# Kernel tuning notes

Measured on AMD Instinct MI355X. Metric: run time of the kernel, lower is better.

## Reference

```python
import jax, jax.numpy as jnp
import numpy as np

N_NODES = 50000
N_EDGES = 500000
D_IN = 256
D_OUT = 256


def setup_inputs() -> dict:
    key = jax.random.key(0)
    ks = jax.random.split(key, 16)
    inp = {
        "features": jax.random.normal(ks[0], (N_NODES, D_IN), dtype=jnp.float32),
        "src0": jax.random.randint(ks[1], (N_EDGES,), 0, N_NODES, dtype=jnp.int64),
        "dst0": jax.random.randint(ks[2], (N_EDGES,), 0, N_NODES, dtype=jnp.int64),
        "src1": jax.random.randint(ks[3], (N_EDGES,), 0, N_NODES, dtype=jnp.int64),
        "dst1": jax.random.randint(ks[4], (N_EDGES,), 0, N_NODES, dtype=jnp.int64),
        "src2": jax.random.randint(ks[5], (N_EDGES,), 0, N_NODES, dtype=jnp.int64),
        "dst2": jax.random.randint(ks[6], (N_EDGES,), 0, N_NODES, dtype=jnp.int64),
    }
    scale = 1.0 / np.sqrt(D_IN)
    for i in range(3):
        inp[f"W{i}"] = jax.random.uniform(ks[7 + 2 * i], (D_IN, D_OUT), dtype=jnp.float32, minval=-scale, maxval=scale)
        inp[f"b{i}"] = jax.random.uniform(ks[8 + 2 * i], (D_OUT,), dtype=jnp.float32, minval=-scale, maxval=scale)
    return inp


def _relation(features, W, b, src, dst, n_nodes):
    # per-relation linear projection: [N, D_out]
    Wh = features @ W + b
    # copy_u: gather projected source features along edges -> [E, D_out]
    msg = Wh[src]
    # mean reduce onto destination nodes
    s = jax.ops.segment_sum(msg, dst, num_segments=n_nodes)
    cnt = jax.ops.segment_sum(jnp.ones((src.shape[0],), features.dtype), dst, num_segments=n_nodes)
    return s / jnp.maximum(cnt, 1.0)[:, None]


def reference(features, src0, dst0, src1, dst1, src2, dst2, W0, b0, W1, b1, W2, b2):
    n = features.shape[0]
    # multi_update_all(..., 'sum'): sum per-relation mean-aggregated messages
    h = (_relation(features, W0, b0, src0, dst0, n)
         + _relation(features, W1, b1, src1, dst1, n)
         + _relation(features, W2, b2, src2, dst2, n))
    return jax.nn.relu(h)
```

## Files before the change

kernel.cpp:

```cpp
#include <hip/hip_runtime.h>
#include <hip/hip_bf16.h>

#define N_NODES 50000
#define N_EDGES 500000
#define D 256
#define N_TOT 768
#define SCAN_N (3 * N_NODES)
#define NMB ((N_NODES + 255) / 256)
#define SLOTS 32
#define OVF_CAP 2048

typedef __attribute__((ext_vector_type(8))) __bf16 bf16x8;
typedef __attribute__((ext_vector_type(4))) float f32x4;

__device__ __forceinline__ unsigned short f2bf(float f) {
    unsigned u = __builtin_bit_cast(unsigned, f);
    u += 0x7FFFu + ((u >> 16) & 1u);
    return (unsigned short)(u >> 16);
}
__device__ __forceinline__ float bf2f(unsigned short h) {
    return __builtin_bit_cast(float, (unsigned)h << 16);
}
__device__ __forceinline__ void gload16(const unsigned short* g, __bf16* l) {
    __builtin_amdgcn_global_load_lds(
        (const __attribute__((address_space(1))) void*)g,
        (__attribute__((address_space(3))) void*)l, 16, 0, 0);
}

__global__ void prep_kernel(const float* __restrict__ feat, unsigned short* __restrict__ fb,
                            const float* __restrict__ W0, const float* __restrict__ W1,
                            const float* __restrict__ W2, unsigned short* __restrict__ WT,
                            const int* __restrict__ s0, const int* __restrict__ d0,
                            const int* __restrict__ s1, const int* __restrict__ d1,
                            const int* __restrict__ s2, const int* __restrict__ d2,
                            int* __restrict__ cur, unsigned short* __restrict__ eidx,
                            int* __restrict__ ovfc, int* __restrict__ ovf) {
    int i = blockIdx.x * blockDim.x + threadIdx.x;
    if (i < N_NODES * D / 4) {
        float4 v = ((const float4*)feat)[i];
        ushort4 pk;
        pk.x = f2bf(v.x); pk.y = f2bf(v.y); pk.z = f2bf(v.z); pk.w = f2bf(v.w);
        ((ushort4*)fb)[i] = pk;
    }
    if (i < N_TOT * D) {
        int j = i >> 8, k = i & 255;
        int r = j >> 8, c = j & 255;
        const float* W = (r == 0) ? W0 : (r == 1) ? W1 : W2;
        WT[i] = f2bf(W[k * D + c]);
    }
    if (i < 3 * N_EDGES) {
        int r = i / N_EDGES;
        int e = i - r * N_EDGES;
        const int* d = (r == 0) ? d0 : (r == 1) ? d1 : d2;
        const int* s = (r == 0) ? s0 : (r == 1) ? s1 : s2;
        int x = r * N_NODES + d[e];
        int rank = atomicAdd(&cur[x], 1);
        if (rank < SLOTS) {
            eidx[(size_t)x * SLOTS + rank] = (unsigned short)s[e];
        } else {
            int op = atomicAdd(ovfc, 1);
            if (op < OVF_CAP) { ovf[2 * op] = x; ovf[2 * op + 1] = s[e]; }
        }
    }
}

__global__ __launch_bounds__(512) void gemm_kernel(
    const unsigned short* __restrict__ A, const unsigned short* __restrict__ BT,
    const float* __restrict__ b0, const float* __restrict__ b1, const float* __restrict__ b2,
    unsigned short* __restrict__ Wh) {
    __shared__ __bf16 Asl[2][256][64];
    __shared__ __bf16 Bsl[2][256][64];
    int tid = threadIdx.x;
    int lane = tid & 63, w = tid >> 6;
    int wr = w >> 2, wc = w & 3;
    int m0 = blockIdx.x * 256;
    int p = blockIdx.y;
    const float* bp = (p == 0) ? b0 : (p == 1) ? b1 : b2;
    f32x4 acc[8][4] = {};

    auto stage = [&](int kt, int b) {
        #pragma unroll
        for (int i = 0; i < 4; ++i) {
            int slot = i * 512 + w * 64 + lane;
            int row = slot >> 3, ks = slot & 7;
            int g = ks ^ (row & 7);
            int gm = m0 + row; if (gm >= N_NODES) gm = N_NODES - 1;
            gload16(A + (size_t)gm * D + kt * 64 + g * 8,
                    &Asl[b][0][0] + (size_t)slot * 8);
            gload16(BT + (size_t)(p * 256 + row) * D + kt * 64 + g * 8,
                    &Bsl[b][0][0] + (size_t)slot * 8);
        }
    };

    stage(0, 0);
    int rr = lane & 15, q = lane >> 4;
    #pragma unroll
    for (int kt = 0; kt < 4; ++kt) {
        asm volatile("s_waitcnt vmcnt(0)" ::: "memory");
        __builtin_amdgcn_s_barrier();
        int b = kt & 1;
        if (kt + 1 < 4) stage(kt + 1, b ^ 1);
        #pragma unroll
        for (int kh = 0; kh < 2; ++kh) {
            bf16x8 af[8], bfr[4];
            #pragma unroll
            for (int mf = 0; mf < 8; ++mf) {
                int row = wr * 128 + mf * 16 + rr;
                int sl = (kh * 4 + q) ^ (row & 7);
                af[mf] = *(const bf16x8*)(&Asl[b][row][0] + sl * 8);
            }
            #pragma unroll
            for (int nf = 0; nf < 4; ++nf) {
                int row = wc * 64 + nf * 16 + rr;
                int sl = (kh * 4 + q) ^ (row & 7);
                bfr[nf] = *(const bf16x8*)(&Bsl[b][row][0] + sl * 8);
            }
            #pragma unroll
            for (int mf = 0; mf < 8; ++mf)
                #pragma unroll
                for (int nf = 0; nf < 4; ++nf)
                    acc[mf][nf] = __builtin_amdgcn_mfma_f32_16x16x32_bf16(af[mf], bfr[nf], acc[mf][nf], 0, 0, 0);
        }
        __builtin_amdgcn_s_barrier();
    }

    #pragma unroll
    for (int mf = 0; mf < 8; ++mf) {
        #pragma unroll
        for (int nf = 0; nf < 4; ++nf) {
            int col = wc * 64 + nf * 16 + rr;
            float bb = bp[col];
            #pragma unroll
            for (int reg = 0; reg < 4; ++reg) {
                int row = m0 + wr * 128 + mf * 16 + q * 4 + reg;
                if (row < N_NODES)
                    Wh[(size_t)row * N_TOT + p * 256 + col] = f2bf(acc[mf][nf][reg] + bb);
            }
        }
    }
}

__global__ void agg_kernel(const unsigned short* __restrict__ Wh, const int* __restrict__ cur,
                           const unsigned short* __restrict__ eidx, const int* __restrict__ ovfc,
                           const int* __restrict__ ovf, float* __restrict__ out) {
    int n = (blockIdx.x * blockDim.x + threadIdx.x) >> 6;
    int lane = threadIdx.x & 63;
    if (n >= N_NODES) return;

    int dg3[3], e3[3];
    #pragma unroll
    for (int r = 0; r < 3; ++r)
        dg3[r] = cur[r * N_NODES + n];
    #pragma unroll
    for (int r = 0; r < 3; ++r) {
        int x = r * N_NODES + n;
        e3[r] = (lane < min(dg3[r], SLOTS)) ? (int)eidx[(size_t)x * SLOTS + lane] : 0;
    }

    float o0 = 0.f, o1 = 0.f, o2 = 0.f, o3 = 0.f;
    #pragma unroll
    for (int r = 0; r < 3; ++r) {
        const unsigned short* whl = Wh + r * 256 + lane * 4;
        int deg = dg3[r];
        int m = min(deg, SLOTS);
        int e = e3[r];
        float4 acc = make_float4(0.f, 0.f, 0.f, 0.f);
        int j = 0;
        for (; j + 7 < m; j += 8) {
            int t0 = __shfl(e, j + 0), t1 = __shfl(e, j + 1), t2 = __shfl(e, j + 2), t3 = __shfl(e, j + 3);
            int t4 = __shfl(e, j + 4), t5 = __shfl(e, j + 5), t6 = __shfl(e, j + 6), t7 = __shfl(e, j + 7);
            ushort4 v0 = *(const ushort4*)(whl + (size_t)t0 * N_TOT);
            ushort4 v1 = *(const ushort4*)(whl + (size_t)t1 * N_TOT);
            ushort4 v2 = *(const ushort4*)(whl + (size_t)t2 * N_TOT);
            ushort4 v3 = *(const ushort4*)(whl + (size_t)t3 * N_TOT);
            ushort4 v4 = *(const ushort4*)(whl + (size_t)t4 * N_TOT);
            ushort4 v5 = *(const ushort4*)(whl + (size_t)t5 * N_TOT);
            ushort4 v6 = *(const ushort4*)(whl + (size_t)t6 * N_TOT);
            ushort4 v7 = *(const ushort4*)(whl + (size_t)t7 * N_TOT);
            acc.x += ((bf2f(v0.x) + bf2f(v1.x)) + (bf2f(v2.x) + bf2f(v3.x))) + ((bf2f(v4.x) + bf2f(v5.x)) + (bf2f(v6.x) + bf2f(v7.x)));
            acc.y += ((bf2f(v0.y) + bf2f(v1.y)) + (bf2f(v2.y) + bf2f(v3.y))) + ((bf2f(v4.y) + bf2f(v5.y)) + (bf2f(v6.y) + bf2f(v7.y)));
            acc.z += ((bf2f(v0.z) + bf2f(v1.z)) + (bf2f(v2.z) + bf2f(v3.z))) + ((bf2f(v4.z) + bf2f(v5.z)) + (bf2f(v6.z) + bf2f(v7.z)));
            acc.w += ((bf2f(v0.w) + bf2f(v1.w)) + (bf2f(v2.w) + bf2f(v3.w))) + ((bf2f(v4.w) + bf2f(v5.w)) + (bf2f(v6.w) + bf2f(v7.w)));
        }
        for (; j < m; ++j) {
            int t = __shfl(e, j);
            ushort4 v = *(const ushort4*)(whl + (size_t)t * N_TOT);
            acc.x += bf2f(v.x); acc.y += bf2f(v.y); acc.z += bf2f(v.z); acc.w += bf2f(v.w);
        }
        if (deg > SLOTS) {
            int x = r * N_NODES + n;
            int nov = min(*ovfc, OVF_CAP);
            for (int i2 = 0; i2 < nov; ++i2) {
                if (ovf[2 * i2] == x) {
                    ushort4 v = *(const ushort4*)(whl + (size_t)ovf[2 * i2 + 1] * N_TOT);
                    acc.x += bf2f(v.x); acc.y += bf2f(v.y); acc.z += bf2f(v.z); acc.w += bf2f(v.w);
                }
            }
        }
        float sc = (deg > 0) ? 1.0f / (float)deg : 0.0f;
        o0 += acc.x * sc; o1 += acc.y * sc; o2 += acc.z * sc; o3 += acc.w * sc;
    }
    f32x4 o;
    o.x = fmaxf(o0, 0.0f); o.y = fmaxf(o1, 0.0f);
    o.z = fmaxf(o2, 0.0f); o.w = fmaxf(o3, 0.0f);
    __builtin_nontemporal_store(o, (f32x4*)(out + (size_t)n * D + lane * 4));
}

extern "C" void kernel_launch(void* const* d_in, const int* in_sizes, int n_in,
                              void* d_out, int out_size, void* d_ws, size_t ws_size,
                              hipStream_t stream) {
    const float* feat = (const float*)d_in[0];
    const int* src0 = (const int*)d_in[1];
    const int* dst0 = (const int*)d_in[2];
    const int* src1 = (const int*)d_in[3];
    const int* dst1 = (const int*)d_in[4];
    const int* src2 = (const int*)d_in[5];
    const int* dst2 = (const int*)d_in[6];
    const float* W0 = (const float*)d_in[7];
    const float* b0 = (const float*)d_in[8];
    const float* W1 = (const float*)d_in[9];
    const float* b1 = (const float*)d_in[10];
    const float* W2 = (const float*)d_in[11];
    const float* b2 = (const float*)d_in[12];
    float* out = (float*)d_out;

    char* ws = (char*)d_ws;
    size_t o = 0;
    auto alloc = [&](size_t bytes) {
        size_t r = o;
        o += (bytes + 255) & ~(size_t)255;
        return r;
    };
    int* cur            = (int*)(ws + alloc((size_t)SCAN_N * 4));
    int* ovfc           = (int*)(ws + alloc(4 + (size_t)OVF_CAP * 8));
    int* ovf            = ovfc + 1;
    unsigned short* eidx = (unsigned short*)(ws + alloc((size_t)SCAN_N * SLOTS * 2));
    unsigned short* WT  = (unsigned short*)(ws + alloc((size_t)N_TOT * D * 2));
    unsigned short* fb  = (unsigned short*)(ws + alloc((size_t)N_NODES * D * 2));
    unsigned short* Wh  = (unsigned short*)(ws + alloc((size_t)N_NODES * N_TOT * 2));

    (void)hipMemsetAsync(cur, 0, (size_t)SCAN_N * 4 + 256, stream);
    prep_kernel<<<(N_NODES * D / 4 + 255) / 256, 256, 0, stream>>>(
        feat, fb, W0, W1, W2, WT,
        src0, dst0, src1, dst1, src2, dst2, cur, eidx, ovfc, ovf);
    dim3 gg(NMB, 3);
    gemm_kernel<<<gg, 512, 0, stream>>>(fb, WT, b0, b1, b2, Wh);
    agg_kernel<<<(N_NODES * 64 + 255) / 256, 256, 0, stream>>>(Wh, cur, eidx, ovfc, ovf, out);
}
```

Before: 271.2 us.

## Overlap edge bucketing with GEMM via extra specialized waves in gemm kernel

The atomic edge-bucketing work moves out of the prep kernel and into four extra wavefronts added to each GEMM workgroup, which grows from 512 to 768 threads. Those extra waves process a contiguous chunk of edge jobs in 8 sub-chunks. After each sub-chunk they issue a barrier, so their barrier count matches the 8 barriers of the MFMA waves. The goal is to hide the latency-bound scattered atomics behind the compute-bound GEMM instead of running them serially in prep. In exchange, the larger workgroup lowers the per-thread register budget for the MFMA waves, which hold large accumulators and may spill. The scheme also relies on both wave groups hitting exactly the same number of barriers.

```diff
diff --git a/kernel.cpp b/kernel.cpp
--- a/kernel.cpp
+++ b/kernel.cpp
@@ -7,6 +7,10 @@
 #define N_TOT 768
 #define SCAN_N (3 * N_NODES)
 #define NMB ((N_NODES + 255) / 256)
+#define NBLK (NMB * 3)
+#define JOBS (3 * N_EDGES)
+#define JPB ((JOBS + NBLK - 1) / NBLK)
+#define CPB ((JPB + 7) / 8)
 #define SLOTS 32
 #define OVF_CAP 2048
 
@@ -29,12 +33,7 @@
 
 __global__ void prep_kernel(const float* __restrict__ feat, unsigned short* __restrict__ fb,
                             const float* __restrict__ W0, const float* __restrict__ W1,
-                            const float* __restrict__ W2, unsigned short* __restrict__ WT,
-                            const int* __restrict__ s0, const int* __restrict__ d0,
-                            const int* __restrict__ s1, const int* __restrict__ d1,
-                            const int* __restrict__ s2, const int* __restrict__ d2,
-                            int* __restrict__ cur, unsigned short* __restrict__ eidx,
-                            int* __restrict__ ovfc, int* __restrict__ ovf) {
+                            const float* __restrict__ W2, unsigned short* __restrict__ WT) {
     int i = blockIdx.x * blockDim.x + threadIdx.x;
     if (i < N_NODES * D / 4) {
         float4 v = ((const float4*)feat)[i];
@@ -48,94 +47,113 @@
         const float* W = (r == 0) ? W0 : (r == 1) ? W1 : W2;
         WT[i] = f2bf(W[k * D + c]);
     }
-    if (i < 3 * N_EDGES) {
-        int r = i / N_EDGES;
-        int e = i - r * N_EDGES;
-        const int* d = (r == 0) ? d0 : (r == 1) ? d1 : d2;
-        const int* s = (r == 0) ? s0 : (r == 1) ? s1 : s2;
-        int x = r * N_NODES + d[e];
-        int rank = atomicAdd(&cur[x], 1);
-        if (rank < SLOTS) {
-            eidx[(size_t)x * SLOTS + rank] = (unsigned short)s[e];
-        } else {
-            int op = atomicAdd(ovfc, 1);
-            if (op < OVF_CAP) { ovf[2 * op] = x; ovf[2 * op + 1] = s[e]; }
-        }
-    }
-}
-
-__global__ __launch_bounds__(512) void gemm_kernel(
+}
+
+__global__ __launch_bounds__(768) void gemm_kernel(
     const unsigned short* __restrict__ A, const unsigned short* __restrict__ BT,
     const float* __restrict__ b0, const float* __restrict__ b1, const float* __restrict__ b2,
-    unsigned short* __restrict__ Wh) {
+    unsigned short* __restrict__ Wh,
+    const int* __restrict__ s0, const int* __restrict__ d0,
+    const int* __restrict__ s1, const int* __restrict__ d1,
+    const int* __restrict__ s2, const int* __restrict__ d2,
+    int* __restrict__ cur, unsigned short* __restrict__ eidx,
+    int* __restrict__ ovfc, int* __restrict__ ovf) {
     __shared__ __bf16 Asl[2][256][64];
     __shared__ __bf16 Bsl[2][256][64];
     int tid = threadIdx.x;
-    int lane = tid & 63, w = tid >> 6;
-    int wr = w >> 2, wc = w & 3;
-    int m0 = blockIdx.x * 256;
-    int p = blockIdx.y;
-    const float* bp = (p == 0) ? b0 : (p == 1) ? b1 : b2;
-    f32x4 acc[8][4] = {};
-
-    auto stage = [&](int kt, int b) {
+    int bid = blockIdx.y * NMB + blockIdx.x;
+
+    if (tid < 512) {
+        int lane = tid & 63, w = tid >> 6;
+        int wr = w >> 2, wc = w & 3;
+        int m0 = blockIdx.x * 256;
+        int p = blockIdx.y;
+        const float* bp = (p == 0) ? b0 : (p == 1) ? b1 : b2;
+        f32x4 acc[8][4] = {};
+
+        auto stage = [&](int kt, int b) {
+            #pragma unroll
+            for (int i = 0; i < 4; ++i) {
+                int slot = i * 512 + w * 64 + lane;
+                int row = slot >> 3, ks = slot & 7;
+                int g = ks ^ (row & 7);
+                int gm = m0 + row; if (gm >= N_NODES) gm = N_NODES - 1;
+                gload16(A + (size_t)gm * D + kt * 64 + g * 8,
+                        &Asl[b][0][0] + (size_t)slot * 8);
+                gload16(BT + (size_t)(p * 256 + row) * D + kt * 64 + g * 8,
+                        &Bsl[b][0][0] + (size_t)slot * 8);
+            }
+        };
+
+        stage(0, 0);
+        int rr = lane & 15, q = lane >> 4;
         #pragma unroll
-        for (int i = 0; i < 4; ++i) {
-            int slot = i * 512 + w * 64 + lane;
-            int row = slot >> 3, ks = slot & 7;
-            int g = ks ^ (row & 7);
-            int gm = m0 + row; if (gm >= N_NODES) gm = N_NODES - 1;
-            gload16(A + (size_t)gm * D + kt * 64 + g * 8,
-                    &Asl[b][0][0] + (size_t)slot * 8);
-            gload16(BT + (size_t)(p * 256 + row) * D + kt * 64 + g * 8,
-                    &Bsl[b][0][0] + (size_t)slot * 8);
-        }
-    };
-
-    stage(0, 0);
-    int rr = lane & 15, q = lane >> 4;
-    #pragma unroll
-    for (int kt = 0; kt < 4; ++kt) {
-        asm volatile("s_waitcnt vmcnt(0)" ::: "memory");
-        __builtin_amdgcn_s_barrier();
-        int b = kt & 1;
-        if (kt + 1 < 4) stage(kt + 1, b ^ 1);
+        for (int kt = 0; kt < 4; ++kt) {
+            asm volatile("s_waitcnt vmcnt(0)" ::: "memory");
+            __builtin_amdgcn_s_barrier();
+            int b = kt & 1;
+            if (kt + 1 < 4) stage(kt + 1, b ^ 1);
+            #pragma unroll
+            for (int kh = 0; kh < 2; ++kh) {
+                bf16x8 af[8], bfr[4];
+                #pragma unroll
+                for (int mf = 0; mf < 8; ++mf) {
+                    int row = wr * 128 + mf * 16 + rr;
+                    int sl = (kh * 4 + q) ^ (row & 7);
+                    af[mf] = *(const bf16x8*)(&Asl[b][row][0] + sl * 8);
+                }
+                #pragma unroll
+                for (int nf = 0; nf < 4; ++nf) {
+                    int row = wc * 64 + nf * 16 + rr;
+                    int sl = (kh * 4 + q) ^ (row & 7);
+                    bfr[nf] = *(const bf16x8*)(&Bsl[b][row][0] + sl * 8);
+                }
+                #pragma unroll
+                for (int mf = 0; mf < 8; ++mf)
+                    #pragma unroll
+                    for (int nf = 0; nf < 4; ++nf)
+                        acc[mf][nf] = __builtin_amdgcn_mfma_f32_16x16x32_bf16(af[mf], bfr[nf], acc[mf][nf], 0, 0, 0);
+            }
+            __builtin_amdgcn_s_barrier();
+        }
+
         #pragma unroll
-        for (int kh = 0; kh < 2; ++kh) {
-            bf16x8 af[8], bfr[4];
-            #pragma unroll
-            for (int mf = 0; mf < 8; ++mf) {
-                int row = wr * 128 + mf * 16 + rr;
-                int sl = (kh * 4 + q) ^ (row & 7);
-                af[mf] = *(const bf16x8*)(&Asl[b][row][0] + sl * 8);
-            }
+        for (int mf = 0; mf < 8; ++mf) {
             #pragma unroll
             for (int nf = 0; nf < 4; ++nf) {
-                int row = wc * 64 + nf * 16 + rr;
-                int sl = (kh * 4 + q) ^ (row & 7);
-                bfr[nf] = *(const bf16x8*)(&Bsl[b][row][0] + sl * 8);
-            }
-            #pragma unroll
-            for (int mf = 0; mf < 8; ++mf)
-                #pragma unroll
-                for (int nf = 0; nf < 4; ++nf)
-                    acc[mf][nf] = __builtin_amdgcn_mfma_f32_16x16x32_bf16(af[mf], bfr[nf], acc[mf][nf], 0, 0, 0);
-        }
-        __builtin_amdgcn_s_barrier();
-    }
-
-    #pragma unroll
-    for (int mf = 0; mf < 8; ++mf) {
-        #pragma unroll
-        for (int nf = 0; nf < 4; ++nf) {
-            int col = wc * 64 + nf * 16 + rr;
-            float bb = bp[col];
-            #pragma unroll
-            for (int reg = 0; reg < 4; ++reg) {
-                int row = m0 + wr * 128 + mf * 16 + q * 4 + reg;
-                if (row < N_NODES)
-                    Wh[(size_t)row * N_TOT + p * 256 + col] = f2bf(acc[mf][nf][reg] + bb);
-            }
+                int col = wc * 64 + nf * 16 + rr;
+                float bb = bp[col];
+                #pragma unroll
+                for (int reg = 0; reg < 4; ++reg) {
+                    int row = m0 + wr * 128 + mf * 16 + q * 4 + reg;
+                    if (row < N_NODES)
+                        Wh[(size_t)row * N_TOT + p * 256 + col] = f2bf(acc[mf][nf][reg] + bb);
+                }
+            }
+        }
+    } else {
+        int ft = tid - 512;
+        int jb0 = bid * JPB;
+        int jend = jb0 + JPB; if (jend > JOBS) jend = JOBS;
+        #pragma unroll 1
+        for (int c = 0; c < 8; ++c) {
+            int cs = jb0 + c * CPB;
+            int ce = cs + CPB; if (ce > jend) ce = jend;
+            for (int j = cs + ft; j < ce; j += 256) {
+                int r = j / N_EDGES;
+                int e = j - r * N_EDGES;
+                const int* d = (r == 0) ? d0 : (r == 1) ? d1 : d2;
+                const int* s = (r == 0) ? s0 : (r == 1) ? s1 : s2;
+                int x = r * N_NODES + d[e];
+                int rank = atomicAdd(&cur[x], 1);
+                if (rank < SLOTS) {
+                    eidx[(size_t)x * SLOTS + rank] = (unsigned short)s[e];
+                } else {
+                    int op = atomicAdd(ovfc, 1);
+                    if (op < OVF_CAP) { ovf[2 * op] = x; ovf[2 * op + 1] = s[e]; }
+                }
+            }
+            __builtin_amdgcn_s_barrier();
         }
     }
 }
@@ -240,10 +258,10 @@
     unsigned short* Wh  = (unsigned short*)(ws + alloc((size_t)N_NODES * N_TOT * 2));
 
     (void)hipMemsetAsync(cur, 0, (size_t)SCAN_N * 4 + 256, stream);
-    prep_kernel<<<(N_NODES * D / 4 + 255) / 256, 256, 0, stream>>>(
-        feat, fb, W0, W1, W2, WT,
-        src0, dst0, src1, dst1, src2, dst2, cur, eidx, ovfc, ovf);
+    prep_kernel<<<(N_NODES * D / 4 + 255) / 256, 256, 0, stream>>>(feat, fb, W0, W1, W2, WT);
     dim3 gg(NMB, 3);
-    gemm_kernel<<<gg, 512, 0, stream>>>(fb, WT, b0, b1, b2, Wh);
+    gemm_kernel<<<gg, 768, 0, stream>>>(fb, WT, b0, b1, b2, Wh,
+                                        src0, dst0, src1, dst1, src2, dst2,
+                                        cur, eidx, ovfc, ovf);
     agg_kernel<<<(N_NODES * 64 + 255) / 256, 256, 0, stream>>>(Wh, cur, eidx, ovfc, ovf, out);
 }
```

Measured after the change: 248.4 us. -8.4%, faster.

## Overlap edge bucketing with GEMM by interleaving scatter blocks into GEMM grid

Applied to the files above, without the earlier changes.

Moves the atomic edge-bucketing work out of the prep kernel and into the GEMM launch. Two of every three blocks run a grid-stride loop doing the bucketing, while the remaining blocks do GEMM tiles. The atomic scatter, which is latency bound, can then overlap with compute-bound GEMM tiles. In exchange, the scatter blocks hold the GEMM kernel's large LDS allocation and 512-thread footprint, which can lower GEMM occupancy.

```diff
diff --git a/kernel.cpp b/kernel.cpp
--- a/kernel.cpp
+++ b/kernel.cpp
@@ -7,6 +7,10 @@
 #define N_TOT 768
 #define SCAN_N (3 * N_NODES)
 #define NMB ((N_NODES + 255) / 256)
+#define GBLK (NMB * 3)
+#define FBLK (GBLK * 2)
+#define TBLK (GBLK * 3)
+#define JOBS (3 * N_EDGES)
 #define SLOTS 32
 #define OVF_CAP 2048
 
@@ -29,12 +33,7 @@
 
 __global__ void prep_kernel(const float* __restrict__ feat, unsigned short* __restrict__ fb,
                             const float* __restrict__ W0, const float* __restrict__ W1,
-                            const float* __restrict__ W2, unsigned short* __restrict__ WT,
-                            const int* __restrict__ s0, const int* __restrict__ d0,
-                            const int* __restrict__ s1, const int* __restrict__ d1,
-                            const int* __restrict__ s2, const int* __restrict__ d2,
-                            int* __restrict__ cur, unsigned short* __restrict__ eidx,
-                            int* __restrict__ ovfc, int* __restrict__ ovf) {
+                            const float* __restrict__ W2, unsigned short* __restrict__ WT) {
     int i = blockIdx.x * blockDim.x + threadIdx.x;
     if (i < N_NODES * D / 4) {
         float4 v = ((const float4*)feat)[i];
@@ -48,33 +47,46 @@
         const float* W = (r == 0) ? W0 : (r == 1) ? W1 : W2;
         WT[i] = f2bf(W[k * D + c]);
     }
-    if (i < 3 * N_EDGES) {
-        int r = i / N_EDGES;
-        int e = i - r * N_EDGES;
-        const int* d = (r == 0) ? d0 : (r == 1) ? d1 : d2;
-        const int* s = (r == 0) ? s0 : (r == 1) ? s1 : s2;
-        int x = r * N_NODES + d[e];
-        int rank = atomicAdd(&cur[x], 1);
-        if (rank < SLOTS) {
-            eidx[(size_t)x * SLOTS + rank] = (unsigned short)s[e];
-        } else {
-            int op = atomicAdd(ovfc, 1);
-            if (op < OVF_CAP) { ovf[2 * op] = x; ovf[2 * op + 1] = s[e]; }
-        }
-    }
 }
 
 __global__ __launch_bounds__(512) void gemm_kernel(
     const unsigned short* __restrict__ A, const unsigned short* __restrict__ BT,
     const float* __restrict__ b0, const float* __restrict__ b1, const float* __restrict__ b2,
-    unsigned short* __restrict__ Wh) {
+    unsigned short* __restrict__ Wh,
+    const int* __restrict__ s0, const int* __restrict__ d0,
+    const int* __restrict__ s1, const int* __restrict__ d1,
+    const int* __restrict__ s2, const int* __restrict__ d2,
+    int* __restrict__ cur, unsigned short* __restrict__ eidx,
+    int* __restrict__ ovfc, int* __restrict__ ovf) {
     __shared__ __bf16 Asl[2][256][64];
     __shared__ __bf16 Bsl[2][256][64];
+    int id = blockIdx.x;
     int tid = threadIdx.x;
+
+    if (id % 3 != 0) {
+        int fid = 2 * (id / 3) + (id % 3) - 1;
+        for (int j = fid * 512 + tid; j < JOBS; j += FBLK * 512) {
+            int r = j / N_EDGES;
+            int e = j - r * N_EDGES;
+            const int* d = (r == 0) ? d0 : (r == 1) ? d1 : d2;
+            const int* s = (r == 0) ? s0 : (r == 1) ? s1 : s2;
+            int x = r * N_NODES + d[e];
+            int rank = atomicAdd(&cur[x], 1);
+            if (rank < SLOTS) {
+                eidx[(size_t)x * SLOTS + rank] = (unsigned short)s[e];
+            } else {
+                int op = atomicAdd(ovfc, 1);
+                if (op < OVF_CAP) { ovf[2 * op] = x; ovf[2 * op + 1] = s[e]; }
+            }
+        }
+        return;
+    }
+
+    int g = id / 3;
     int lane = tid & 63, w = tid >> 6;
     int wr = w >> 2, wc = w & 3;
-    int m0 = blockIdx.x * 256;
-    int p = blockIdx.y;
+    int m0 = (g % NMB) * 256;
+    int p = g / NMB;
     const float* bp = (p == 0) ? b0 : (p == 1) ? b1 : b2;
     f32x4 acc[8][4] = {};
 
@@ -83,11 +95,11 @@
         for (int i = 0; i < 4; ++i) {
             int slot = i * 512 + w * 64 + lane;
             int row = slot >> 3, ks = slot & 7;
-            int g = ks ^ (row & 7);
+            int gsl = ks ^ (row & 7);
             int gm = m0 + row; if (gm >= N_NODES) gm = N_NODES - 1;
-            gload16(A + (size_t)gm * D + kt * 64 + g * 8,
+            gload16(A + (size_t)gm * D + kt * 64 + gsl * 8,
                     &Asl[b][0][0] + (size_t)slot * 8);
-            gload16(BT + (size_t)(p * 256 + row) * D + kt * 64 + g * 8,
+            gload16(BT + (size_t)(p * 256 + row) * D + kt * 64 + gsl * 8,
                     &Bsl[b][0][0] + (size_t)slot * 8);
         }
     };
@@ -240,10 +252,9 @@
     unsigned short* Wh  = (unsigned short*)(ws + alloc((size_t)N_NODES * N_TOT * 2));
 
     (void)hipMemsetAsync(cur, 0, (size_t)SCAN_N * 4 + 256, stream);
-    prep_kernel<<<(N_NODES * D / 4 + 255) / 256, 256, 0, stream>>>(
-        feat, fb, W0, W1, W2, WT,
-        src0, dst0, src1, dst1, src2, dst2, cur, eidx, ovfc, ovf);
-    dim3 gg(NMB, 3);
-    gemm_kernel<<<gg, 512, 0, stream>>>(fb, WT, b0, b1, b2, Wh);
+    prep_kernel<<<(N_NODES * D / 4 + 255) / 256, 256, 0, stream>>>(feat, fb, W0, W1, W2, WT);
+    gemm_kernel<<<TBLK, 512, 0, stream>>>(fb, WT, b0, b1, b2, Wh,
+                                          src0, dst0, src1, dst1, src2, dst2,
+                                          cur, eidx, ovfc, ovf);
     agg_kernel<<<(N_NODES * 64 + 255) / 256, 256, 0, stream>>>(Wh, cur, eidx, ovfc, ovf, out);
 }
```

After: 222.6 us. 1.22x faster.
